# Kernel optimization log

Measured on AMD Instinct MI355X. Metric: run time of the kernel, lower is better.

## Reference

```python
import jax, jax.numpy as jnp
import numpy as np

D_MODEL = 2048
N_HEADS = 16
N_KV = 4
D_HEAD = D_MODEL // N_HEADS  # 128
KERNEL = 4
TOTAL_QKV = (N_HEADS + 2 * N_KV) * D_HEAD  # 3072
BATCH, SEQ = 2, 2048


def setup_inputs() -> dict:
    key = jax.random.key(0)
    ks = jax.random.split(key, 6)
    s = 1.0 / np.sqrt(D_MODEL)
    return {
        "hidden_states": jax.random.normal(ks[0], (BATCH, SEQ, D_MODEL), jnp.float32),
        "w_q": jax.random.normal(ks[1], (D_MODEL, N_HEADS * D_HEAD), jnp.float32) * s,
        "w_k": jax.random.normal(ks[2], (D_MODEL, N_KV * D_HEAD), jnp.float32) * s,
        "w_v": jax.random.normal(ks[3], (D_MODEL, N_KV * D_HEAD), jnp.float32) * s,
        "w_o": jax.random.normal(ks[4], (N_HEADS * D_HEAD, D_MODEL), jnp.float32) * s,
        "conv_w": jax.random.normal(ks[5], (TOTAL_QKV, KERNEL), jnp.float32) * 0.1,
    }


def _canon_b(x, conv_w):
    """Depthwise causal conv1d with residual. x: [B,S,C], conv_w: [C,K]."""
    K = conv_w.shape[1]
    xp = jnp.pad(x, ((0, 0), (K - 1, 0), (0, 0)))  # left pad for causality
    S = x.shape[1]
    out = sum(xp[:, k:k + S, :] * conv_w[:, k] for k in range(K))
    return x + out


def reference(hidden_states, w_q, w_k, w_v, w_o, conv_w):
    B, S, _ = hidden_states.shape
    q = hidden_states @ w_q   # [B,S,Hq*Dh]
    k = hidden_states @ w_k   # [B,S,Hkv*Dh]
    v = hidden_states @ w_v
    qkv = jnp.concatenate([q, k, v], axis=-1)
    qkv = _canon_b(qkv, conv_w)
    q_dim = N_HEADS * D_HEAD
    kv_dim = N_KV * D_HEAD
    q, k, v = jnp.split(qkv, [q_dim, q_dim + kv_dim], axis=-1)
    q = q.reshape(B, S, N_HEADS, D_HEAD)
    k = k.reshape(B, S, N_KV, D_HEAD)
    v = v.reshape(B, S, N_KV, D_HEAD)
    # GQA: repeat kv heads to match query heads
    groups = N_HEADS // N_KV
    k = jnp.repeat(k, groups, axis=2)
    v = jnp.repeat(v, groups, axis=2)
    scale = 1.0 / np.sqrt(D_HEAD)
    scores = jnp.einsum("bqhd,bkhd->bhqk", q, k) * scale  # [B,H,S,S]
    causal = jnp.tril(jnp.ones((S, S), dtype=bool))
    scores = jnp.where(causal, scores, jnp.finfo(scores.dtype).min)
    probs = jax.nn.softmax(scores, axis=-1)
    attended = jnp.einsum("bhqk,bkhd->bqhd", probs, v)  # [B,S,H,Dh]
    attended = attended.reshape(B, S, N_HEADS * D_HEAD)
    return attended @ w_o
```

## Files before the change

kernel.cpp:

```cpp
#include <hip/hip_runtime.h>
#include <stdint.h>

typedef unsigned short u16;
typedef short short8 __attribute__((ext_vector_type(8)));
typedef float f32x4 __attribute__((ext_vector_type(4)));
typedef float f32x16 __attribute__((ext_vector_type(16)));

#define DM    2048
#define NH    16
#define NKV   4
#define DH    128
#define TQKV  3072
#define NB    2
#define SEQL  2048
#define MROWS (NB * SEQL)
#define QDIM  (NH * DH)
#define KVDIM (NKV * DH)
#define QSCALE_L2E 0.1275174336f

#define MFMA16(a, b, c) __builtin_amdgcn_mfma_f32_16x16x32_bf16((a), (b), (c), 0, 0, 0)
#define MFMA32(a, b, c) __builtin_amdgcn_mfma_f32_32x32x16_bf16((a), (b), (c), 0, 0, 0)

__device__ __forceinline__ u16 f2bf(float f) {
  uint32_t u = __float_as_uint(f);
  u += 0x7fffu + ((u >> 16) & 1u);
  return (u16)(u >> 16);
}
__device__ __forceinline__ float bf2f(u16 h) {
  return __uint_as_float(((uint32_t)h) << 16);
}
__device__ __forceinline__ void gload16(const u16* g, u16* l) {
  __builtin_amdgcn_global_load_lds((__attribute__((address_space(1))) void*)(u16*)g,
                                   (__attribute__((address_space(3))) void*)l, 16, 0, 0);
}
__device__ __forceinline__ uint32_t cvtpk(float lo, float hi) {
  uint32_t r;
  asm("v_cvt_pk_bf16_f32 %0, %1, %2" : "=v"(r) : "v"(lo), "v"(hi));
  return r;
}
__device__ __forceinline__ void swapln(uint32_t& a, uint32_t& b) {
  asm volatile("v_permlane32_swap_b32 %0, %1" : "+v"(a), "+v"(b));
}

__global__ void k_f32_to_bf16(const float* __restrict__ src, u16* __restrict__ dst, int n) {
  int i = (blockIdx.x * blockDim.x + threadIdx.x) * 4;
  if (i >= n) return;
  float4 v = *reinterpret_cast<const float4*>(src + i);
  u16 o0 = f2bf(v.x), o1 = f2bf(v.y), o2 = f2bf(v.z), o3 = f2bf(v.w);
  u16* d = dst + i;
  d[0] = o0; d[1] = o1; d[2] = o2; d[3] = o3;
}

__global__ void k_transpose_f32_bf16(const float* __restrict__ src, u16* __restrict__ dst,
                                     int K, int N, int rowOff, int dstLd) {
  __shared__ float t[32][33];
  const int n0 = blockIdx.x * 32, k0 = blockIdx.y * 32;
  const int tx = threadIdx.x, ty = threadIdx.y;
#pragma unroll
  for (int i = ty; i < 32; i += 8)
    t[i][tx] = src[(size_t)(k0 + i) * N + (n0 + tx)];
  __syncthreads();
#pragma unroll
  for (int i = ty; i < 32; i += 8)
    dst[(size_t)(rowOff + n0 + i) * dstLd + (k0 + tx)] = f2bf(t[tx][i]);
}

__global__ void k_transpose_bf16(const u16* __restrict__ src, u16* __restrict__ dst, int R, int C) {
  __shared__ u16 t[32][33];
  const size_t zoff = (size_t)blockIdx.z * R * C;
  const int c0 = blockIdx.x * 32, r0 = blockIdx.y * 32;
  const int tx = threadIdx.x, ty = threadIdx.y;
#pragma unroll
  for (int i = ty; i < 32; i += 8)
    t[i][tx] = src[zoff + (size_t)(r0 + i) * C + (c0 + tx)];
  __syncthreads();
#pragma unroll
  for (int i = ty; i < 32; i += 8)
    dst[zoff + (size_t)(c0 + i) * R + (r0 + tx)] = t[tx][i];
}

template <int OUTBF>
__global__ __launch_bounds__(256) void k_gemm_bt(const u16* __restrict__ A, const u16* __restrict__ Bt,
                                                 float* __restrict__ Cf, u16* __restrict__ Cb,
                                                 int M, int N, int K) {
  __shared__ u16 As[2][128 * 32];
  __shared__ u16 Bs[2][128 * 32];
  const int tid = threadIdx.x;
  const int m0 = blockIdx.x * 128;
  const int n0 = blockIdx.y * 128;
  const int r  = tid >> 2;
  const int c8 = (tid & 3) << 3;
  const u16* Ag0 = A  + (size_t)(m0 + r) * K + c8;
  const u16* Ag1 = A  + (size_t)(m0 + 64 + r) * K + c8;
  const u16* Bg0 = Bt + (size_t)(n0 + r) * K + c8;
  const u16* Bg1 = Bt + (size_t)(n0 + 64 + r) * K + c8;

  auto stage = [&](int buf, int kt) {
    const int kg = kt * 32;
    gload16(Ag0 + kg, &As[buf][tid * 8]);
    gload16(Ag1 + kg, &As[buf][2048 + tid * 8]);
    gload16(Bg0 + kg, &Bs[buf][tid * 8]);
    gload16(Bg1 + kg, &Bs[buf][2048 + tid * 8]);
  };

  f32x4 acc[4][4];
#pragma unroll
  for (int i = 0; i < 4; ++i)
#pragma unroll
    for (int j = 0; j < 4; ++j) acc[i][j] = (f32x4){0.f, 0.f, 0.f, 0.f};

  const int wv = tid >> 6, ln = tid & 63;
  const int wr = (wv >> 1) * 64, wc = (wv & 1) * 64;
  const int lr = ln & 15, lko = (ln >> 4) * 8;

  stage(0, 0);
  __syncthreads();

  const int nk = K >> 5;
  for (int kt = 0; kt < nk; ++kt) {
    const int cur = kt & 1;
    if (kt + 1 < nk) stage(cur ^ 1, kt + 1);
    short8 af[4], bf[4];
#pragma unroll
    for (int i = 0; i < 4; ++i)
      af[i] = *reinterpret_cast<const short8*>(&As[cur][(wr + i * 16 + lr) * 32 + lko]);
#pragma unroll
    for (int i = 0; i < 4; ++i)
      bf[i] = *reinterpret_cast<const short8*>(&Bs[cur][(wc + i * 16 + lr) * 32 + lko]);
#pragma unroll
    for (int i = 0; i < 4; ++i)
#pragma unroll
      for (int j = 0; j < 4; ++j)
        acc[i][j] = MFMA16(af[i], bf[j], acc[i][j]);
    __syncthreads();
  }

  const int rg = (ln >> 4) * 4;
#pragma unroll
  for (int i = 0; i < 4; ++i) {
#pragma unroll
    for (int j = 0; j < 4; ++j) {
      const int row = m0 + wr + i * 16 + rg;
      const int col = n0 + wc + j * 16 + lr;
#pragma unroll
      for (int q = 0; q < 4; ++q) {
        float v = acc[i][j][q];
        if (OUTBF) Cb[(size_t)(row + q) * N + col] = f2bf(v);
        else       Cf[(size_t)(row + q) * N + col] = v;
      }
    }
  }
}

__global__ void k_conv_route(const u16* __restrict__ qkv, const float* __restrict__ cw,
                             u16* __restrict__ Qh, u16* __restrict__ Kh, u16* __restrict__ Vsd) {
  const int row = blockIdx.x;
  const int b = row >> 11, s = row & 2047;
  const int c = threadIdx.x * 8;
  float x[4][8];
#pragma unroll
  for (int k = 0; k < 4; ++k) {
    const int sr = s + k - 3;
    if (sr < 0) {
#pragma unroll
      for (int j = 0; j < 8; ++j) x[k][j] = 0.f;
    } else {
      short8 v = *reinterpret_cast<const short8*>(&qkv[(size_t)(b * SEQL + sr) * TQKV + c]);
#pragma unroll
      for (int j = 0; j < 8; ++j) x[k][j] = bf2f((u16)v[j]);
    }
  }
  float o[8];
#pragma unroll
  for (int j = 0; j < 8; ++j) {
    float4 w4 = *reinterpret_cast<const float4*>(&cw[(c + j) * 4]);
    o[j] = x[3][j] + x[0][j] * w4.x + x[1][j] * w4.y + x[2][j] * w4.z + x[3][j] * w4.w;
  }
  short8 ov;
  if (c < QDIM) {
#pragma unroll
    for (int j = 0; j < 8; ++j) ov[j] = (short)f2bf(o[j] * QSCALE_L2E);
    const int h = c >> 7, d = c & 127;
    *reinterpret_cast<short8*>(&Qh[((size_t)(b * NH + h) * SEQL + s) * DH + d]) = ov;
  } else if (c < QDIM + KVDIM) {
#pragma unroll
    for (int j = 0; j < 8; ++j) ov[j] = (short)f2bf(o[j]);
    const int cc = c - QDIM;
    const int h = cc >> 7, d = cc & 127;
    *reinterpret_cast<short8*>(&Kh[((size_t)(b * NKV + h) * SEQL + s) * DH + d]) = ov;
  } else {
#pragma unroll
    for (int j = 0; j < 8; ++j) ov[j] = (short)f2bf(o[j]);
    const int cc = c - QDIM - KVDIM;
    const int h = cc >> 7, d = cc & 127;
    *reinterpret_cast<short8*>(&Vsd[((size_t)(b * NKV + h) * SEQL + s) * DH + d]) = ov;
  }
}

__global__ __launch_bounds__(512) void k_attn(const u16* __restrict__ Qh, const u16* __restrict__ Kh,
                                              const u16* __restrict__ Vt, u16* __restrict__ att,
                                              u16* __restrict__ pO, float* __restrict__ pm,
                                              float* __restrict__ pl) {
  static const int qbA_t[8] = {7,6,5,4,7,6,5,4};
  static const int tA0_t[8] = {0,0,0,0,18,18,18,18};
  static const int tA1_t[8] = {18,18,18,18,32,28,24,20};
  static const int chkA_t[8]= {0,0,0,0,1,1,1,1};
  static const int qbB_t[8] = {0,0,0,0,0,1,2,3};
  static const int tB1_t[8] = {0,0,0,0,4,8,12,16};

  const int slot = blockIdx.x >> 5;
  const int bh = blockIdx.x & 31;
  const int s = bh & 7, tt = bh >> 3;
  const int b = s >> 2, kvh = s & 3;
  const int h = kvh * 4 + tt;
  const int bhl = b * NH + h;

  __shared__ u16 Ks[2][64 * 128];
  __shared__ u16 Vs[2][128 * 64];
  const int tid = threadIdx.x, wv = tid >> 6, ln = tid & 63;
  const int lq = ln & 31, hi = ln >> 5;
  const int hi16 = hi * 16;
  const int swr = (lq & 7) << 4;

  const u16* kg = Kh + (size_t)(b * NKV + kvh) * SEQL * DH;
  const u16* vg = Vt + (size_t)(b * NKV + kvh) * DH * SEQL;

  const int ck0 = tid, ck1 = tid + 512;
  const int krow0 = ck0 >> 4, kcb0 = (ck0 & 15) << 4;
  const int krow1 = ck1 >> 4, kcb1 = (ck1 & 15) << 4;
  const int koff0 = krow0 * DH + ((kcb0 ^ ((krow0 & 7) << 4)) >> 1);
  const int koff1 = krow1 * DH + ((kcb1 ^ ((krow1 & 7) << 4)) >> 1);
  const int vd0 = ck0 >> 3, vcb0 = (ck0 & 7) << 4;
  const int vd1 = ck1 >> 3, vcb1 = (ck1 & 7) << 4;
  const int voff0 = vd0 * SEQL + ((vcb0 ^ ((vd0 & 7) << 4)) >> 1);
  const int voff1 = vd1 * SEQL + ((vcb1 ^ ((vd1 & 7) << 4)) >> 1);

  auto stage = [&](int buf, int kvs) {
    gload16(kg + (size_t)kvs * DH + koff0, &Ks[buf][ck0 * 8]);
    gload16(kg + (size_t)kvs * DH + koff1, &Ks[buf][ck1 * 8]);
    gload16(vg + (size_t)kvs + voff0, &Vs[buf][ck0 * 8]);
    gload16(vg + (size_t)kvs + voff1, &Vs[buf][ck1 * 8]);
  };

  for (int seg = 0; seg < 2; ++seg) {
    int qb, tA, tB, split, chk;
    if (seg == 0) {
      qb = qbA_t[slot]; tA = tA0_t[slot]; tB = tA1_t[slot]; split = 1; chk = chkA_t[slot];
    } else {
      tB = tB1_t[slot];
      if (tB == 0) break;
      qb = qbB_t[slot]; tA = 0; split = 0; chk = 0;
    }

    const int q0w = qb * 256 + wv * 32;
    const int qg = q0w + lq;

    const u16* qrow = Qh + ((size_t)(b * NH + h) * SEQL + qg) * DH;
    short8 qf[8];
#pragma unroll
    for (int dblk = 0; dblk < 8; ++dblk)
      qf[dblk] = *reinterpret_cast<const short8*>(qrow + dblk * 16 + hi * 8);

    f32x16 oacc[4];
#pragma unroll
    for (int nb = 0; nb < 4; ++nb)
#pragma unroll
      for (int rq = 0; rq < 16; ++rq) oacc[nb][rq] = 0.f;
    float mrow = -1e30f, lrow = 0.f;

    stage(0, tA * 64);
    __syncthreads();

    for (int t = tA; t < tB; ++t) {
      const int cur = (t - tA) & 1;
      const int kvs = t * 64;
      if (t + 1 < tB) stage(cur ^ 1, kvs + 64);
      if (kvs <= q0w + 31) {
        const u16* ks = Ks[cur];
        const u16* vs = Vs[cur];
        f32x16 st[2];
#pragma unroll
        for (int kvb = 0; kvb < 2; ++kvb)
#pragma unroll
          for (int rq = 0; rq < 16; ++rq) st[kvb][rq] = 0.f;

        __builtin_amdgcn_s_setprio(1);
#pragma unroll
        for (int kvb = 0; kvb < 2; ++kvb) {
          const u16* krow = ks + (kvb * 32 + lq) * 128;
#pragma unroll
          for (int dblk = 0; dblk < 8; ++dblk) {
            short8 kf = *reinterpret_cast<const short8*>(krow + (((dblk * 32 + hi16) ^ swr) >> 1));
            st[kvb] = MFMA32(kf, qf[dblk], st[kvb]);
          }
        }
        __builtin_amdgcn_s_setprio(0);

        if (kvs + 63 > q0w) {
#pragma unroll
          for (int kvb = 0; kvb < 2; ++kvb)
#pragma unroll
            for (int rq = 0; rq < 16; ++rq) {
              const int kvg = kvs + kvb * 32 + (rq & 3) + 8 * (rq >> 2) + 4 * hi;
              if (kvg > qg) st[kvb][rq] = -1e30f;
            }
        }

        float a0 = st[0][0], a1 = st[0][1], a2 = st[0][2], a3 = st[0][3];
#pragma unroll
        for (int kvb = 0; kvb < 2; ++kvb)
#pragma unroll
          for (int rq = (kvb ? 0 : 4); rq < 16; rq += 4) {
            a0 = fmaxf(a0, st[kvb][rq]);
            a1 = fmaxf(a1, st[kvb][rq + 1]);
            a2 = fmaxf(a2, st[kvb][rq + 2]);
            a3 = fmaxf(a3, st[kvb][rq + 3]);
          }
        float tm = fmaxf(fmaxf(a0, a1), fmaxf(a2, a3));
        tm = fmaxf(tm, __shfl_xor(tm, 32));
        if (__any(tm > mrow + 11.0f)) {
          const float nm = fmaxf(mrow, tm);
          const float scl = exp2f(mrow - nm);
          mrow = nm;
          lrow *= scl;
#pragma unroll
          for (int nb = 0; nb < 4; ++nb)
#pragma unroll
            for (int rq = 0; rq < 16; ++rq) oacc[nb][rq] *= scl;
        }
        float s0 = 0.f, s1 = 0.f, s2 = 0.f, s3 = 0.f;
#pragma unroll
        for (int kvb = 0; kvb < 2; ++kvb)
#pragma unroll
          for (int rq = 0; rq < 16; rq += 4) {
            float p0 = exp2f(st[kvb][rq] - mrow);
            float p1 = exp2f(st[kvb][rq + 1] - mrow);
            float p2 = exp2f(st[kvb][rq + 2] - mrow);
            float p3 = exp2f(st[kvb][rq + 3] - mrow);
            st[kvb][rq] = p0; st[kvb][rq + 1] = p1; st[kvb][rq + 2] = p2; st[kvb][rq + 3] = p3;
            s0 += p0; s1 += p1; s2 += p2; s3 += p3;
          }
        float ps = (s0 + s1) + (s2 + s3);
        ps += __shfl_xor(ps, 32);
        lrow += ps;

        uint32_t w[4][4];
#pragma unroll
        for (int kvb = 0; kvb < 2; ++kvb) {
          uint32_t x0 = cvtpk(st[kvb][0], st[kvb][1]);
          uint32_t y0 = cvtpk(st[kvb][4], st[kvb][5]);
          swapln(x0, y0);
          uint32_t x1 = cvtpk(st[kvb][2], st[kvb][3]);
          uint32_t y1 = cvtpk(st[kvb][6], st[kvb][7]);
          swapln(x1, y1);
          w[kvb * 2][0] = x0; w[kvb * 2][1] = x1; w[kvb * 2][2] = y0; w[kvb * 2][3] = y1;
          uint32_t x2 = cvtpk(st[kvb][8], st[kvb][9]);
          uint32_t y2 = cvtpk(st[kvb][12], st[kvb][13]);
          swapln(x2, y2);
          uint32_t x3 = cvtpk(st[kvb][10], st[kvb][11]);
          uint32_t y3 = cvtpk(st[kvb][14], st[kvb][15]);
          swapln(x3, y3);
          w[kvb * 2 + 1][0] = x2; w[kvb * 2 + 1][1] = x3; w[kvb * 2 + 1][2] = y2; w[kvb * 2 + 1][3] = y3;
        }
        short8 pa[4];
#pragma unroll
        for (int kc = 0; kc < 4; ++kc) {
          union { uint32_t uw[4]; short8 s; } pu;
#pragma unroll
          for (int j = 0; j < 4; ++j) pu.uw[j] = w[kc][j];
          pa[kc] = pu.s;
        }

        __builtin_amdgcn_s_setprio(1);
#pragma unroll
        for (int nb = 0; nb < 4; ++nb) {
          const u16* vrow = vs + (nb * 32 + lq) * 64;
#pragma unroll
          for (int kc = 0; kc < 4; ++kc) {
            short8 vf = *reinterpret_cast<const short8*>(vrow + (((kc * 32 + hi16) ^ swr) >> 1));
            oacc[nb] = MFMA32(vf, pa[kc], oacc[nb]);
          }
        }
        __builtin_amdgcn_s_setprio(0);
      }
      __syncthreads();
    }

    if (!split) {
      const float inv = 1.0f / lrow;
      u16* orow = att + ((size_t)(b * SEQL + qg)) * QDIM + h * DH;
#pragma unroll
      for (int nb = 0; nb < 4; ++nb)
#pragma unroll
        for (int rg = 0; rg < 4; ++rg) {
          const int rq = rg * 4;
          uint2 vout;
          vout.x = cvtpk(oacc[nb][rq] * inv, oacc[nb][rq + 1] * inv);
          vout.y = cvtpk(oacc[nb][rq + 2] * inv, oacc[nb][rq + 3] * inv);
          *reinterpret_cast<uint2*>(orow + nb * 32 + 8 * rg + 4 * hi) = vout;
        }
    } else {
      const int rowp = ((bhl * 4 + (qb - 4)) << 8) + wv * 32 + lq;
      u16* prow = pO + (size_t)chk * 32768 * 128 + (size_t)rowp * 128;
#pragma unroll
      for (int nb = 0; nb < 4; ++nb)
#pragma unroll
        for (int rg = 0; rg < 4; ++rg) {
          const int rq = rg * 4;
          uint2 vout;
          vout.x = cvtpk(oacc[nb][rq], oacc[nb][rq + 1]);
          vout.y = cvtpk(oacc[nb][rq + 2], oacc[nb][rq + 3]);
          *reinterpret_cast<uint2*>(prow + nb * 32 + 8 * rg + 4 * hi) = vout;
        }
      if (!hi) {
        pm[chk * 32768 + rowp] = mrow;
        pl[chk * 32768 + rowp] = lrow;
      }
    }
    __syncthreads();
  }
}

__global__ void k_combine(const u16* __restrict__ pO, const float* __restrict__ pm,
                          const float* __restrict__ pl, u16* __restrict__ att) {
  const int e = blockIdx.x * 256 + threadIdx.x;
  const int rowp = e >> 4;
  const int d8 = (e & 15) * 8;
  const float m0 = pm[rowp], m1 = pm[32768 + rowp];
  const float l0 = pl[rowp], l1 = pl[32768 + rowp];
  const float mm = fmaxf(m0, m1);
  const float a0 = exp2f(m0 - mm), a1 = exp2f(m1 - mm);
  const float inv = 1.0f / (l0 * a0 + l1 * a1);
  const float w0 = a0 * inv, w1 = a1 * inv;
  short8 o0 = *reinterpret_cast<const short8*>(pO + (size_t)rowp * 128 + d8);
  short8 o1 = *reinterpret_cast<const short8*>(pO + (size_t)32768 * 128 + (size_t)rowp * 128 + d8);
  const int bh = rowp >> 10, qb = 4 + ((rowp >> 8) & 3), r = rowp & 255;
  const int b = bh >> 4, h = bh & 15;
  u16* orow = att + ((size_t)(b * SEQL + qb * 256 + r)) * QDIM + h * DH + d8;
  uint2 vout;
  float r0 = bf2f((u16)o0[0]) * w0 + bf2f((u16)o1[0]) * w1;
  float r1 = bf2f((u16)o0[1]) * w0 + bf2f((u16)o1[1]) * w1;
  float r2 = bf2f((u16)o0[2]) * w0 + bf2f((u16)o1[2]) * w1;
  float r3 = bf2f((u16)o0[3]) * w0 + bf2f((u16)o1[3]) * w1;
  float r4 = bf2f((u16)o0[4]) * w0 + bf2f((u16)o1[4]) * w1;
  float r5 = bf2f((u16)o0[5]) * w0 + bf2f((u16)o1[5]) * w1;
  float r6 = bf2f((u16)o0[6]) * w0 + bf2f((u16)o1[6]) * w1;
  float r7 = bf2f((u16)o0[7]) * w0 + bf2f((u16)o1[7]) * w1;
  vout.x = ((uint32_t)f2bf(r1) << 16) | f2bf(r0);
  vout.y = ((uint32_t)f2bf(r3) << 16) | f2bf(r2);
  uint2 vout2;
  vout2.x = ((uint32_t)f2bf(r5) << 16) | f2bf(r4);
  vout2.y = ((uint32_t)f2bf(r7) << 16) | f2bf(r6);
  *reinterpret_cast<uint2*>(orow) = vout;
  *reinterpret_cast<uint2*>(orow + 4) = vout2;
}

extern "C" void kernel_launch(void* const* d_in, const int* in_sizes, int n_in,
                              void* d_out, int out_size, void* d_ws, size_t ws_size,
                              hipStream_t stream) {
  const float* hin = (const float*)d_in[0];
  const float* wq  = (const float*)d_in[1];
  const float* wk  = (const float*)d_in[2];
  const float* wvv = (const float*)d_in[3];
  const float* wo  = (const float*)d_in[4];
  const float* cw  = (const float*)d_in[5];
  float* out = (float*)d_out;
  char* ws = (char*)d_ws;

  u16* h_bf = (u16*)(ws + 0);
  u16* Wt   = (u16*)(ws + 16777216);
  u16* Wot  = (u16*)(ws + 29360128);
  u16* Qh   = (u16*)(ws + 37748736);
  u16* Kh   = (u16*)(ws + 54525952);
  u16* Vsd  = (u16*)(ws + 58720256);
  u16* Vt   = (u16*)(ws + 62914560);
  u16* att  = (u16*)(ws + 67108864);
  u16* qkv  = (u16*)d_out;
  u16*   pO = (u16*)d_out;
  float* pm = (float*)((char*)d_out + 16777216);
  float* pl = (float*)((char*)d_out + 16777216 + 262144);

  dim3 tb(32, 8);
  k_f32_to_bf16<<<8192, 256, 0, stream>>>(hin, h_bf, MROWS * DM);
  k_transpose_f32_bf16<<<dim3(64, 64), tb, 0, stream>>>(wq, Wt, 2048, 2048, 0, 2048);
  k_transpose_f32_bf16<<<dim3(16, 64), tb, 0, stream>>>(wk, Wt, 2048, 512, 2048, 2048);
  k_transpose_f32_bf16<<<dim3(16, 64), tb, 0, stream>>>(wvv, Wt, 2048, 512, 2560, 2048);
  k_transpose_f32_bf16<<<dim3(64, 64), tb, 0, stream>>>(wo, Wot, 2048, 2048, 0, 2048);
  k_gemm_bt<1><<<dim3(32, 24), 256, 0, stream>>>(h_bf, Wt, nullptr, qkv, MROWS, TQKV, DM);
  k_conv_route<<<MROWS, 384, 0, stream>>>(qkv, cw, Qh, Kh, Vsd);
  k_transpose_bf16<<<dim3(4, 64, NB * NKV), tb, 0, stream>>>(Vsd, Vt, SEQL, DH);
  k_attn<<<dim3(256), 512, 0, stream>>>(Qh, Kh, Vt, att, pO, pm, pl);
  k_combine<<<dim3(2048), 256, 0, stream>>>(pO, pm, pl, att);
  k_gemm_bt<0><<<dim3(32, 16), 256, 0, stream>>>(att, Wot, out, nullptr, MROWS, DM, DM);
}
```

Before: 237.4 us.

## Triple-buffer attention KV staging and fuse input prep kernels into one launch

The attention loop moves from double to triple-buffered K/V shared-memory staging with a prefetch distance of two tiles. It replaces the two full barriers per iteration with an explicit vmcnt wait and a single barrier, to hide global load latency. The bf16 cast of hidden states and the four weight transposes are merged into one kernel launch to cut launch overhead. LDS use rises to 96 KB per block, and correctness depends on the hand-written vmcnt count matching the loads issued per stage.

```diff
diff --git a/kernel.cpp b/kernel.cpp
--- a/kernel.cpp
+++ b/kernel.cpp
@@ -42,27 +42,38 @@
   asm volatile("v_permlane32_swap_b32 %0, %1" : "+v"(a), "+v"(b));
 }
 
-__global__ void k_f32_to_bf16(const float* __restrict__ src, u16* __restrict__ dst, int n) {
-  int i = (blockIdx.x * blockDim.x + threadIdx.x) * 4;
-  if (i >= n) return;
-  float4 v = *reinterpret_cast<const float4*>(src + i);
-  u16 o0 = f2bf(v.x), o1 = f2bf(v.y), o2 = f2bf(v.z), o3 = f2bf(v.w);
-  u16* d = dst + i;
-  d[0] = o0; d[1] = o1; d[2] = o2; d[3] = o3;
-}
-
-__global__ void k_transpose_f32_bf16(const float* __restrict__ src, u16* __restrict__ dst,
-                                     int K, int N, int rowOff, int dstLd) {
+__global__ __launch_bounds__(256) void k_prep(const float* __restrict__ hin,
+                                              const float* __restrict__ wq,
+                                              const float* __restrict__ wk,
+                                              const float* __restrict__ wvv,
+                                              const float* __restrict__ wo,
+                                              u16* __restrict__ h_bf,
+                                              u16* __restrict__ Wt,
+                                              u16* __restrict__ Wot) {
   __shared__ float t[32][33];
-  const int n0 = blockIdx.x * 32, k0 = blockIdx.y * 32;
-  const int tx = threadIdx.x, ty = threadIdx.y;
+  const int bid = blockIdx.x;
+  const int tid = threadIdx.x;
+  if (bid < 8192) {
+    const int i = (bid * 256 + tid) * 4;
+    float4 v = *reinterpret_cast<const float4*>(hin + i);
+    u16* d = h_bf + i;
+    d[0] = f2bf(v.x); d[1] = f2bf(v.y); d[2] = f2bf(v.z); d[3] = f2bf(v.w);
+    return;
+  }
+  const float* src; u16* dst; int N, rowOff, bx, by;
+  if (bid < 12288)      { const int r = bid - 8192;  src = wq;  dst = Wt;  N = 2048; rowOff = 0;    bx = r & 63; by = r >> 6; }
+  else if (bid < 13312) { const int r = bid - 12288; src = wk;  dst = Wt;  N = 512;  rowOff = 2048; bx = r & 15; by = r >> 4; }
+  else if (bid < 14336) { const int r = bid - 13312; src = wvv; dst = Wt;  N = 512;  rowOff = 2560; bx = r & 15; by = r >> 4; }
+  else                  { const int r = bid - 14336; src = wo;  dst = Wot; N = 2048; rowOff = 0;    bx = r & 63; by = r >> 6; }
+  const int n0 = bx * 32, k0 = by * 32;
+  const int tx = tid & 31, ty = tid >> 5;
 #pragma unroll
   for (int i = ty; i < 32; i += 8)
     t[i][tx] = src[(size_t)(k0 + i) * N + (n0 + tx)];
   __syncthreads();
 #pragma unroll
   for (int i = ty; i < 32; i += 8)
-    dst[(size_t)(rowOff + n0 + i) * dstLd + (k0 + tx)] = f2bf(t[tx][i]);
+    dst[(size_t)(rowOff + n0 + i) * 2048 + (k0 + tx)] = f2bf(t[tx][i]);
 }
 
 __global__ void k_transpose_bf16(const u16* __restrict__ src, u16* __restrict__ dst, int R, int C) {
@@ -215,8 +226,8 @@
   const int h = kvh * 4 + tt;
   const int bhl = b * NH + h;
 
-  __shared__ u16 Ks[2][64 * 128];
-  __shared__ u16 Vs[2][128 * 64];
+  __shared__ u16 Ks[3][64 * 128];
+  __shared__ u16 Vs[3][128 * 64];
   const int tid = threadIdx.x, wv = tid >> 6, ln = tid & 63;
   const int lq = ln & 31, hi = ln >> 5;
   const int hi16 = hi * 16;
@@ -269,12 +280,17 @@
     float mrow = -1e30f, lrow = 0.f;
 
     stage(0, tA * 64);
-    __syncthreads();
+    if (tA + 1 < tB) stage(1, (tA + 1) * 64);
+    int cur = 0;
 
     for (int t = tA; t < tB; ++t) {
-      const int cur = (t - tA) & 1;
+      if (t + 1 < tB) { asm volatile("s_waitcnt vmcnt(4)" ::: "memory"); }
+      else            { asm volatile("s_waitcnt vmcnt(0)" ::: "memory"); }
+      __builtin_amdgcn_s_barrier();
+      const int nxt = (cur == 2) ? 0 : cur + 1;
+      const int nn  = (nxt == 2) ? 0 : nxt + 1;
+      if (t + 2 < tB) stage(nn, (t + 2) * 64);
       const int kvs = t * 64;
-      if (t + 1 < tB) stage(cur ^ 1, kvs + 64);
       if (kvs <= q0w + 31) {
         const u16* ks = Ks[cur];
         const u16* vs = Vs[cur];
@@ -383,7 +399,7 @@
         }
         __builtin_amdgcn_s_setprio(0);
       }
-      __syncthreads();
+      cur = nxt;
     }
 
     if (!split) {
@@ -481,11 +497,7 @@
   float* pl = (float*)((char*)d_out + 16777216 + 262144);
 
   dim3 tb(32, 8);
-  k_f32_to_bf16<<<8192, 256, 0, stream>>>(hin, h_bf, MROWS * DM);
-  k_transpose_f32_bf16<<<dim3(64, 64), tb, 0, stream>>>(wq, Wt, 2048, 2048, 0, 2048);
-  k_transpose_f32_bf16<<<dim3(16, 64), tb, 0, stream>>>(wk, Wt, 2048, 512, 2048, 2048);
-  k_transpose_f32_bf16<<<dim3(16, 64), tb, 0, stream>>>(wvv, Wt, 2048, 512, 2560, 2048);
-  k_transpose_f32_bf16<<<dim3(64, 64), tb, 0, stream>>>(wo, Wot, 2048, 2048, 0, 2048);
+  k_prep<<<dim3(18432), 256, 0, stream>>>(hin, wq, wk, wvv, wo, h_bf, Wt, Wot);
   k_gemm_bt<1><<<dim3(32, 24), 256, 0, stream>>>(h_bf, Wt, nullptr, qkv, MROWS, TQKV, DM);
   k_conv_route<<<MROWS, 384, 0, stream>>>(qkv, cw, Qh, Kh, Vsd);
   k_transpose_bf16<<<dim3(4, 64, NB * NKV), tb, 0, stream>>>(Vsd, Vt, SEQL, DH);
```

Result: faster. 227.4 us (-4.2%).
